# Kernel optimization log

Measured on AMD Instinct MI355X. Metric: run time of the kernel, lower is better.

## Reference

```python
import jax, jax.numpy as jnp
import numpy as np
from jax import lax

K = 3; PAD = 1; STR = 1; DIL = 1; DG = 16; MRM = 10.0


def _conv3(x, w, b):
    y = lax.conv_general_dilated(x, w, (1, 1), ((PAD, PAD), (PAD, PAD)),
                                 dimension_numbers=('NCHW', 'OIHW', 'NCHW'))
    return y + b[None, :, None, None]


def _leaky(x):
    return jnp.where(x >= 0, x, 0.1 * x)


def _bilinear_gather(img, py, px):
    # img: [B, dg, cg, H, W]; py, px: [B, dg, KK, H, W] sampling coords
    B, dg, cg, H, W = img.shape
    KK = py.shape[2]
    y0f = jnp.floor(py); x0f = jnp.floor(px)
    wy = py - y0f; wx = px - x0f          # bilinear fractions (grad flows via py/px)
    y0 = y0f.astype(jnp.int32); x0 = x0f.astype(jnp.int32)
    y1 = y0 + 1; x1 = x0 + 1
    imgf = img.reshape(B * dg, cg, H * W)

    def gather(yi, xi):
        valid = ((yi >= 0) & (yi < H) & (xi >= 0) & (xi < W)).astype(img.dtype)
        idx = jnp.clip(yi, 0, H - 1) * W + jnp.clip(xi, 0, W - 1)
        idxf = idx.reshape(B * dg, KK * H * W)
        v = jax.vmap(lambda im, ix: im[:, ix])(imgf, idxf)  # [B*dg, cg, KK*H*W]
        v = v.reshape(B, dg, cg, KK, H, W)
        return v * valid[:, :, None]  # zero padding outside image

    w00 = ((1 - wy) * (1 - wx))[:, :, None]
    w01 = ((1 - wy) * wx)[:, :, None]
    w10 = (wy * (1 - wx))[:, :, None]
    w11 = (wy * wx)[:, :, None]
    return (gather(y0, x0) * w00 + gather(y0, x1) * w01 +
            gather(y1, x0) * w10 + gather(y1, x1) * w11)


def reference(x, extra_feat, flow, w1, b1, w2, b2, w3, b3, weight):
    B, C, H, W = x.shape
    KK = K * K
    cg = C // DG
    P = DG * KK
    # offset/mask generating convnet
    h = _leaky(_conv3(extra_feat, w1, b1))
    h = _leaky(_conv3(h, w2, b2))
    o = _conv3(h, w3, b3)                       # [B, 3*P, H, W]
    o1, o2, m = jnp.split(o, 3, axis=1)
    off = MRM * jnp.tanh(jnp.concatenate([o1, o2], axis=1))  # [B, 2P, H, W]
    flow_yx = flow[:, ::-1]                      # flip(1): (x,y)->(y,x)
    off = off + jnp.tile(flow_yx, (1, P, 1, 1))
    off = off.reshape(B, DG, KK, 2, H, W)        # pair p=(g,k): channel 2p=y, 2p+1=x
    off_y = off[:, :, :, 0]
    off_x = off[:, :, :, 1]
    mask = jax.nn.sigmoid(m).reshape(B, DG, KK, H, W)

    ki = jnp.arange(KK)
    ky = (ki // K).astype(x.dtype) * DIL - PAD   # kernel row offsets
    kx = (ki % K).astype(x.dtype) * DIL - PAD
    base_h = jnp.arange(H, dtype=x.dtype) * STR
    base_w = jnp.arange(W, dtype=x.dtype) * STR
    py = base_h[None, None, None, :, None] + ky[None, None, :, None, None] + off_y
    px = base_w[None, None, None, None, :] + kx[None, None, :, None, None] + off_x

    img = x.reshape(B, DG, cg, H, W)
    val = _bilinear_gather(img, py, px) * mask[:, :, None]  # [B,dg,cg,KK,H,W]
    wk = weight.reshape(weight.shape[0], DG, cg, KK)
    # modulated deformable conv accumulate (bias=None in original forward)
    return jnp.einsum('bgckhw,ogck->bohw', val, wk)


def setup_inputs() -> dict:
    key = jax.random.key(0)
    ks = jax.random.split(key, 10)
    B, C, H, W = 2, 64, 128, 128
    OFFC = 3 * K * K * DG  # 432
    return {
        'x': jax.random.normal(ks[0], (B, C, H, W), jnp.float32),
        'extra_feat': jax.random.normal(ks[1], (B, 2 * C, H, W), jnp.float32),
        'flow': jax.random.normal(ks[2], (B, 2, H, W), jnp.float32),
        'w1': jax.random.normal(ks[3], (C, 2 * C, 3, 3), jnp.float32) * 0.05,
        'b1': jnp.zeros((C,), jnp.float32),
        'w2': jax.random.normal(ks[4], (C, C, 3, 3), jnp.float32) * 0.05,
        'b2': jnp.zeros((C,), jnp.float32),
        'w3': jax.random.normal(ks[5], (OFFC, C, 3, 3), jnp.float32) * 0.01,
        'b3': jnp.zeros((OFFC,), jnp.float32),
        'weight': jax.random.normal(ks[6], (C, C, 3, 3), jnp.float32) * 0.05,
    }
```

## Files before the change

### kernel.cpp

```cpp
#include <hip/hip_runtime.h>
#include <math.h>

constexpr int B_   = 2;
constexpr int C_   = 64;
constexpr int H_   = 128;
constexpr int W_   = 128;
constexpr int HW_  = H_ * W_;
constexpr int DG_  = 16;
constexpr int KK_  = 9;
constexpr int CG_  = 4;
constexpr int OFFC_ = 3 * KK_ * DG_;
constexpr int R_   = C_ * KK_;
constexpr int WP_  = 130;
constexpr int HWP_ = WP_ * WP_;

typedef _Float16 half8 __attribute__((ext_vector_type(8)));
typedef _Float16 half4 __attribute__((ext_vector_type(4)));
typedef float floatx4 __attribute__((ext_vector_type(4)));

__device__ __forceinline__ void gl_lds16(const _Float16* g, _Float16* l)
{
    __builtin_amdgcn_global_load_lds(
        (const __attribute__((address_space(1))) void*)g,
        (__attribute__((address_space(3))) void*)l, 16, 0, 0);
}

__device__ __forceinline__ int afrag_src(int c)
{
    const int cmf = c >> 6, cq = (c >> 4) & 3, cl = c & 15;
    return (cmf * 16 + cl) * 32 + cq * 8;
}

template <int OC, int CIN>
__global__ __launch_bounds__(256) void prep_wA_k(
    const float* __restrict__ w, _Float16* __restrict__ wA)
{
    constexpr int CH = CIN / 32;
    const int j = blockIdx.x * 256 + threadIdx.x;
    if (j >= 9 * CH * OC * 32) return;
    const int slab = j / (OC * 32);
    const int rem  = j - slab * (OC * 32);
    const int oc   = rem >> 5;
    const int jj   = rem & 31;
    const int t    = slab / CH;
    const int h    = slab - t * CH;
    const int ic   = h * 32 + jj;
    wA[j] = (_Float16)w[(size_t)oc * (CIN * 9) + ic * 9 + t];
}

__global__ __launch_bounds__(256) void prep_wkA_k(
    const float* __restrict__ wk, _Float16* __restrict__ wkA)
{
    const int j = blockIdx.x * 256 + threadIdx.x;
    if (j >= 18 * 64 * 32) return;
    const int s   = j >> 11;
    const int rem = j & 2047;
    const int oc  = rem >> 5;
    const int jj  = rem & 31;
    const int k   = s >> 1;
    const int gc  = (s & 1) * 32 + jj;
    wkA[j] = (_Float16)wk[(size_t)oc * R_ + gc * 9 + k];
}

template <int CC>
__global__ __launch_bounds__(256) void nchw2slabpad_f16_k(
    const float* __restrict__ in, _Float16* __restrict__ outh)
{
    const int pix = blockIdx.x * 256 + threadIdx.x;
    const int b   = blockIdx.y;
    const int yp  = pix >> 7;
    const int xp  = pix & (W_ - 1);
    const float* ib = in + (size_t)b * CC * HW_ + pix;
#pragma unroll
    for (int c0 = 0; c0 < CC; c0 += 8) {
        half8 v;
#pragma unroll
        for (int j = 0; j < 8; ++j)
            v[j] = (_Float16)ib[(size_t)(c0 + j) * HW_];
        const int slab = c0 >> 5;
        *(half8*)&outh[((size_t)(slab * B_ + b) * HWP_
                        + (size_t)(yp + 1) * WP_ + (xp + 1)) * 32 + (c0 & 31)] = v;
    }
}

__global__ __launch_bounds__(256) void nchw2gx_f16_k(
    const float* __restrict__ in, _Float16* __restrict__ outh)
{
    const int pix = blockIdx.x * 256 + threadIdx.x;
    const int b   = blockIdx.y;
    const float* ib = in + (size_t)b * C_ * HW_ + pix;
#pragma unroll
    for (int g = 0; g < DG_; ++g) {
        half4 v;
#pragma unroll
        for (int c = 0; c < 4; ++c)
            v[c] = (_Float16)ib[(size_t)(g * 4 + c) * HW_];
        *(half4*)&outh[((size_t)(b * DG_ + g) * HW_ + pix) * 4] = v;
    }
}

template <int CIN>
__global__ __launch_bounds__(256, 2) void conv12_mfma_k(
    const _Float16* __restrict__ inp, const _Float16* __restrict__ wA,
    const float* __restrict__ bias, _Float16* __restrict__ outp)
{
    constexpr int CH = CIN / 32;
    constexpr int NS = 9 * CH;
    __shared__ __align__(16) _Float16 Asm[2 * 2048];

    const int tid  = threadIdx.x;
    const int lane = tid & 63;
    const int wv   = tid >> 6;
    const int l15  = lane & 15;
    const int quad = lane >> 4;

    const int zx   = blockIdx.x;
    const int row  = zx >> 1;
    const int b    = row >> 7;
    const int y    = row & 127;
    const int px0  = (zx & 1) * 64 + wv * 16;

    const int sA = afrag_src(tid);

    floatx4 acc[4];
#pragma unroll
    for (int mf = 0; mf < 4; ++mf)
        acc[mf] = (floatx4){0.f, 0.f, 0.f, 0.f};

    half8 Bf[2];

    gl_lds16(wA + sA, Asm + tid * 8);
    Bf[0] = *(const half8*)&inp[
        ((size_t)(0 * B_ + b) * HWP_ + (size_t)(y + 0) * WP_
         + (px0 + l15 + 0)) * 32 + quad * 8];
    __syncthreads();

#pragma unroll
    for (int ks = 0; ks < NS; ++ks) {
        const int cur = ks & 1, nxt = cur ^ 1;
        if (ks < NS - 1) {
            const int ks1 = ks + 1;
            const int t = ks1 / CH, h = ks1 % CH;
            const int dy = t / 3, dx = t % 3;
            gl_lds16(wA + (size_t)ks1 * 2048 + sA, Asm + nxt * 2048 + tid * 8);
            Bf[nxt] = *(const half8*)&inp[
                ((size_t)(h * B_ + b) * HWP_ + (size_t)(y + dy) * WP_
                 + (px0 + l15 + dx)) * 32 + quad * 8];
        }
        const _Float16* abase = Asm + cur * 2048 + lane * 8;
#pragma unroll
        for (int mf = 0; mf < 4; ++mf) {
            const half8 afr = *(const half8*)&abase[mf * 512];
            acc[mf] = __builtin_amdgcn_mfma_f32_16x16x32_f16(afr, Bf[cur], acc[mf], 0, 0, 0);
        }
        __syncthreads();
    }

#pragma unroll
    for (int mf = 0; mf < 4; ++mf) {
        const int oc4 = mf * 16 + quad * 4;
        const float4 b4 = *(const float4*)&bias[oc4];
        half4 v4;
#pragma unroll
        for (int reg = 0; reg < 4; ++reg) {
            float r = acc[mf][reg] + ((const float*)&b4)[reg];
            r = (r >= 0.f) ? r : 0.1f * r;
            v4[reg] = (_Float16)r;
        }
        *(half4*)&outp[((size_t)((oc4 >> 5) * B_ + b) * HWP_
                        + (size_t)(y + 1) * WP_ + (px0 + l15 + 1)) * 32 + (oc4 & 31)] = v4;
    }
}

__global__ __launch_bounds__(256, 2) void conv3_mfma_k(
    const _Float16* __restrict__ h2p, const _Float16* __restrict__ w3A,
    const float* __restrict__ bias, const float* __restrict__ flow,
    _Float16* __restrict__ omh)
{
    __shared__ __align__(16) _Float16 Smem[144 * 132];
    _Float16* Asm = Smem;
    _Float16* Lds = Smem;

    const int tid  = threadIdx.x;
    const int lane = tid & 63;
    const int wv   = tid >> 6;
    const int l15  = lane & 15;
    const int quad = lane >> 4;

    const int row = blockIdx.x;
    const int b   = row >> 7;
    const int y   = row & 127;
    const int m0  = blockIdx.y * 144;
    const int px0 = wv * 32;

    const int c0 = wv * 64 + lane;
    const int c1 = 256 + c0;
    const int c2 = 512 + lane;
    const int s0 = afrag_src(c0), s1 = afrag_src(c1), s2 = afrag_src(c2);

    floatx4 acc[9][2];
#pragma unroll
    for (int mf = 0; mf < 9; ++mf)
#pragma unroll
        for (int nf = 0; nf < 2; ++nf)
            acc[mf][nf] = (floatx4){0.f, 0.f, 0.f, 0.f};

    half8 Bf[2][2];

    {
        const _Float16* asrc = w3A + (size_t)m0 * 32;
        gl_lds16(asrc + s0, Asm + c0 * 8);
        gl_lds16(asrc + s1, Asm + c1 * 8);
        if (wv == 0) gl_lds16(asrc + s2, Asm + c2 * 8);
#pragma unroll
        for (int nf = 0; nf < 2; ++nf)
            Bf[0][nf] = *(const half8*)&h2p[
                ((size_t)(0 * B_ + b) * HWP_ + (size_t)(y + 0) * WP_
                 + (px0 + nf * 16 + l15 + 0)) * 32 + quad * 8];
    }
    __syncthreads();

#pragma unroll
    for (int ks = 0; ks < 18; ++ks) {
        const int cur = ks & 1, nxt = cur ^ 1;
        if (ks < 17) {
            const int ks1 = ks + 1;
            const int t = ks1 >> 1, h = ks1 & 1;
            const int dy = t / 3, dx = t % 3;
            const _Float16* asrc = w3A + ((size_t)ks1 * OFFC_ + m0) * 32;
            _Float16* adst = Asm + nxt * 4608;
            gl_lds16(asrc + s0, adst + c0 * 8);
            gl_lds16(asrc + s1, adst + c1 * 8);
            if (wv == 0) gl_lds16(asrc + s2, adst + c2 * 8);
#pragma unroll
            for (int nf = 0; nf < 2; ++nf)
                Bf[nxt][nf] = *(const half8*)&h2p[
                    ((size_t)(h * B_ + b) * HWP_ + (size_t)(y + dy) * WP_
                     + (px0 + nf * 16 + l15 + dx)) * 32 + quad * 8];
        }
        const _Float16* abase = Asm + cur * 4608 + lane * 8;
#pragma unroll
        for (int mf = 0; mf < 9; ++mf) {
            const half8 afr = *(const half8*)&abase[mf * 512];
            acc[mf][0] = __builtin_amdgcn_mfma_f32_16x16x32_f16(afr, Bf[cur][0], acc[mf][0], 0, 0, 0);
            acc[mf][1] = __builtin_amdgcn_mfma_f32_16x16x32_f16(afr, Bf[cur][1], acc[mf][1], 0, 0, 0);
        }
        __syncthreads();
    }

    const bool is_off = (blockIdx.y < 2);
    float flY[2], flX[2];
#pragma unroll
    for (int nf = 0; nf < 2; ++nf) {
        const int px = px0 + nf * 16 + l15;
        if (is_off) {
            flY[nf] = flow[(size_t)(b * 2 + 1) * HW_ + y * W_ + px];
            flX[nf] = flow[(size_t)(b * 2 + 0) * HW_ + y * W_ + px];
        }
    }
#pragma unroll
    for (int mf = 0; mf < 9; ++mf) {
        const float4 b4 = *(const float4*)&bias[m0 + mf * 16 + quad * 4];
#pragma unroll
        for (int nf = 0; nf < 2; ++nf) {
            const int px = px0 + nf * 16 + l15;
#pragma unroll
            for (int reg = 0; reg < 4; ++reg) {
                const int ocl = mf * 16 + quad * 4 + reg;
                float val = acc[mf][nf][reg] + ((const float*)&b4)[reg];
                if (is_off) {
                    const int slot = reg & 1;
                    const float fl = slot ? flX[nf] : flY[nf];
                    const float e = __expf(2.f * val);
                    val = 10.f * (1.f - __fdividef(2.f, e + 1.f)) + fl;
                } else {
                    val = __fdividef(1.f, 1.f + __expf(-val));
                }
                Lds[ocl * 132 + px] = (_Float16)val;
            }
        }
    }
    __syncthreads();

#pragma unroll
    for (int it = 0; it < 18; ++it) {
        const int j4 = it * 256 + tid;
        const int r  = j4 >> 5;
        const int c4 = j4 & 31;
        const int oc = m0 + r;
        int g, k, slot;
        if (oc < 2 * DG_ * KK_) {
            g = oc / 18;
            const int rem = oc - g * 18;
            k = rem >> 1;
            slot = rem & 1;
        } else {
            const int c = oc - 2 * DG_ * KK_;
            g = c / 9;
            k = c - g * 9;
            slot = 2;
        }
        const half4 hv = *(const half4*)&Lds[r * 132 + c4 * 4];
        *(half4*)&omh[((size_t)((b * DG_ * KK_ + g * KK_ + k) * 3 + slot)) * HW_
                      + y * W_ + c4 * 4] = hv;
    }
}

__global__ __launch_bounds__(256) void gather_k(
    const _Float16* __restrict__ xg, const _Float16* __restrict__ omh,
    _Float16* __restrict__ valh)
{
    const int tid = threadIdx.x;
    const int pix = blockIdx.x * 256 + tid;
    const int zy  = blockIdx.y;
    const int b   = zy / KK_;
    const int k   = zy - b * KK_;
    const int yp  = pix >> 7;
    const int xp  = pix & (W_ - 1);
    const float fy = (float)(yp + (k / 3) - 1);
    const float fx = (float)(xp + (k % 3) - 1);

    half4 rec[16];
#pragma unroll
    for (int g = 0; g < DG_; ++g) {
        const size_t obase = ((size_t)((b * DG_ + g) * KK_ + k) * 3) * HW_ + pix;
        const float oy = (float)omh[obase];
        const float ox = (float)omh[obase + HW_];
        const float m  = (float)omh[obase + 2 * HW_];

        const float py = fy + oy;
        const float px = fx + ox;
        const float y0f = floorf(py);
        const float x0f = floorf(px);
        const float wy = py - y0f;
        const float wx = px - x0f;
        const int y0 = (int)y0f, x0 = (int)x0f;
        const int y1 = y0 + 1,  x1 = x0 + 1;
        const bool vy0 = ((unsigned)y0 < (unsigned)H_);
        const bool vy1 = ((unsigned)y1 < (unsigned)H_);
        const bool vx0 = ((unsigned)x0 < (unsigned)W_);
        const bool vx1 = ((unsigned)x1 < (unsigned)W_);
        const float w00 = vy0 && vx0 ? (1.f - wy) * (1.f - wx) : 0.f;
        const float w01 = vy0 && vx1 ? (1.f - wy) * wx         : 0.f;
        const float w10 = vy1 && vx0 ? wy * (1.f - wx)         : 0.f;
        const float w11 = vy1 && vx1 ? wy * wx                 : 0.f;
        const int i00 = (vy0 && vx0) ? y0 * W_ + x0 : 0;
        const int i01 = (vy0 && vx1) ? y0 * W_ + x1 : 0;
        const int i10 = (vy1 && vx0) ? y1 * W_ + x0 : 0;
        const int i11 = (vy1 && vx1) ? y1 * W_ + x1 : 0;

        const _Float16* xb = xg + (size_t)(b * DG_ + g) * HW_ * 4;
        const half4 p00 = *(const half4*)&xb[(size_t)i00 * 4];
        const half4 p01 = *(const half4*)&xb[(size_t)i01 * 4];
        const half4 p10 = *(const half4*)&xb[(size_t)i10 * 4];
        const half4 p11 = *(const half4*)&xb[(size_t)i11 * 4];

        half4 v4;
#pragma unroll
        for (int c = 0; c < CG_; ++c) {
            float v = w00 * (float)p00[c] + w01 * (float)p01[c]
                    + w10 * (float)p10[c] + w11 * (float)p11[c];
            v4[c] = (_Float16)(v * m);
        }
        rec[g] = v4;
    }

    _Float16* r0 = &valh[((size_t)((2 * k) * B_ + b) * HW_ + pix) * 32];
    _Float16* r1 = &valh[((size_t)((2 * k + 1) * B_ + b) * HW_ + pix) * 32];
#pragma unroll
    for (int j = 0; j < 4; ++j) {
        half8 w0, w1;
#pragma unroll
        for (int c = 0; c < 4; ++c) {
            w0[c]     = rec[2 * j][c];
            w0[c + 4] = rec[2 * j + 1][c];
            w1[c]     = rec[8 + 2 * j][c];
            w1[c + 4] = rec[9 + 2 * j][c];
        }
        *(half8*)&r0[j * 8] = w0;
        *(half8*)&r1[j * 8] = w1;
    }
}

__global__ __launch_bounds__(256, 2) void einsum_mfma_k(
    const _Float16* __restrict__ valh, const _Float16* __restrict__ wkA,
    float* __restrict__ out)
{
    __shared__ __align__(16) float Smem[64 * 68];
    _Float16* Asm = (_Float16*)Smem;
    float*    Lds = Smem;

    const int tid  = threadIdx.x;
    const int lane = tid & 63;
    const int wv   = tid >> 6;
    const int l15  = lane & 15;
    const int quad = lane >> 4;

    const int pixg0 = blockIdx.x * 64 + wv * 16;
    const int b     = pixg0 >> 14;
    const int pix0  = pixg0 & (HW_ - 1);

    const int sA = afrag_src(tid);

    floatx4 acc[4];
#pragma unroll
    for (int mf = 0; mf < 4; ++mf)
        acc[mf] = (floatx4){0.f, 0.f, 0.f, 0.f};

    half8 Bf[2];

    gl_lds16(wkA + sA, Asm + tid * 8);
    Bf[0] = *(const half8*)&valh[((size_t)(0 * B_ + b) * HW_ + pix0 + l15) * 32 + quad * 8];
    __syncthreads();

#pragma unroll
    for (int s = 0; s < 18; ++s) {
        const int cur = s & 1, nxt = cur ^ 1;
        if (s < 17) {
            const int s1 = s + 1;
            gl_lds16(wkA + (size_t)s1 * 2048 + sA, Asm + nxt * 2048 + tid * 8);
            Bf[nxt] = *(const half8*)&valh[
                ((size_t)(s1 * B_ + b) * HW_ + pix0 + l15) * 32 + quad * 8];
        }
        const _Float16* abase = Asm + cur * 2048 + lane * 8;
#pragma unroll
        for (int mf = 0; mf < 4; ++mf) {
            const half8 afr = *(const half8*)&abase[mf * 512];
            acc[mf] = __builtin_amdgcn_mfma_f32_16x16x32_f16(afr, Bf[cur], acc[mf], 0, 0, 0);
        }
        __syncthreads();
    }

    const int pxl = wv * 16 + l15;
#pragma unroll
    for (int mf = 0; mf < 4; ++mf)
#pragma unroll
        for (int reg = 0; reg < 4; ++reg)
            Lds[(mf * 16 + quad * 4 + reg) * 68 + pxl] = acc[mf][reg];
    __syncthreads();

    const int pixb = blockIdx.x * 64 & (HW_ - 1);
#pragma unroll
    for (int it = 0; it < 4; ++it) {
        const int j4 = it * 256 + tid;
        const int r  = j4 >> 4;
        const int c4 = j4 & 15;
        float4 v;
        v.x = Lds[r * 68 + c4 * 4 + 0];
        v.y = Lds[r * 68 + c4 * 4 + 1];
        v.z = Lds[r * 68 + c4 * 4 + 2];
        v.w = Lds[r * 68 + c4 * 4 + 3];
        *(float4*)&out[((size_t)(b * C_ + r)) * HW_ + pixb + c4 * 4] = v;
    }
}

extern "C" void kernel_launch(void* const* d_in, const int* in_sizes, int n_in,
                              void* d_out, int out_size, void* d_ws, size_t ws_size,
                              hipStream_t stream)
{
    const float* x    = (const float*)d_in[0];
    const float* ef   = (const float*)d_in[1];
    const float* flow = (const float*)d_in[2];
    const float* w1   = (const float*)d_in[3];
    const float* b1   = (const float*)d_in[4];
    const float* w2   = (const float*)d_in[5];
    const float* b2   = (const float*)d_in[6];
    const float* w3   = (const float*)d_in[7];
    const float* b3   = (const float*)d_in[8];
    const float* wk   = (const float*)d_in[9];
    float* out = (float*)d_out;

    _Float16* omh  = (_Float16*)d_ws;
    _Float16* valh = omh + (size_t)B_ * OFFC_ * HW_;
    _Float16* ef_p = valh + (size_t)18 * B_ * HW_ * 32;
    _Float16* xg   = ef_p + (size_t)4 * B_ * HWP_ * 32;
    _Float16* h1p  = xg + (size_t)B_ * HW_ * 64;
    _Float16* h2p  = h1p + (size_t)2 * B_ * HWP_ * 32;
    _Float16* w1A  = h2p + (size_t)2 * B_ * HWP_ * 32;
    _Float16* w2A  = w1A + 64 * 128 * 9;
    _Float16* w3A  = w2A + 64 * 64 * 9;
    _Float16* wkA  = w3A + OFFC_ * 64 * 9;

    hipMemsetAsync(ef_p, 0, (size_t)4 * B_ * HWP_ * 32 * 2, stream);
    hipMemsetAsync(h1p, 0, (size_t)2 * B_ * HWP_ * 32 * 2, stream);
    hipMemsetAsync(h2p, 0, (size_t)2 * B_ * HWP_ * 32 * 2, stream);

    prep_wA_k<64, 128><<<dim3((64 * 128 * 9 + 255) / 256), 256, 0, stream>>>(w1, w1A);
    prep_wA_k<64, 64><<<dim3((64 * 64 * 9 + 255) / 256), 256, 0, stream>>>(w2, w2A);
    prep_wA_k<OFFC_, 64><<<dim3((OFFC_ * 64 * 9 + 255) / 256), 256, 0, stream>>>(w3, w3A);
    prep_wkA_k<<<dim3((18 * 64 * 32 + 255) / 256), 256, 0, stream>>>(wk, wkA);
    nchw2slabpad_f16_k<128><<<dim3(HW_ / 256, B_), 256, 0, stream>>>(ef, ef_p);
    nchw2gx_f16_k<<<dim3(HW_ / 256, B_), 256, 0, stream>>>(x, xg);

    conv12_mfma_k<128><<<dim3(B_ * H_ * 2), 256, 0, stream>>>(ef_p, w1A, b1, h1p);
    conv12_mfma_k<64><<<dim3(B_ * H_ * 2), 256, 0, stream>>>(h1p, w2A, b2, h2p);
    conv3_mfma_k<<<dim3(B_ * H_, 3), 256, 0, stream>>>(h2p, w3A, b3, flow, omh);

    gather_k<<<dim3(HW_ / 256, B_ * KK_), 256, 0, stream>>>(xg, omh, valh);
    einsum_mfma_k<<<dim3(B_ * HW_ / 64), 256, 0, stream>>>(valh, wkA, out);
}
```

Measured before the change: 204.8 us.

## Cut barriers in conv and einsum kernels via wider stages and resident weights

Conv1 and conv3 now process two K-slices per pipeline stage, which halves the number of __syncthreads barriers and doubles the prefetch depth. Conv2 and the einsum kernel preload all 18 weight slices into LDS up front and drop the per-step barriers, so only the activation loads stay double-buffered. This trades more LDS per block (up to 72 KB, and a larger conv3 staging area) and possibly fewer resident blocks for less synchronisation overhead in the MFMA loops.

```diff
diff --git a/kernel.cpp b/kernel.cpp
--- a/kernel.cpp
+++ b/kernel.cpp
@@ -99,14 +99,11 @@
     }
 }
 
-template <int CIN>
-__global__ __launch_bounds__(256, 2) void conv12_mfma_k(
+__global__ __launch_bounds__(256, 2) void conv1_mfma_k(
     const _Float16* __restrict__ inp, const _Float16* __restrict__ wA,
     const float* __restrict__ bias, _Float16* __restrict__ outp)
 {
-    constexpr int CH = CIN / 32;
-    constexpr int NS = 9 * CH;
-    __shared__ __align__(16) _Float16 Asm[2 * 2048];
+    __shared__ __align__(16) _Float16 Asm[2 * 4096];
 
     const int tid  = threadIdx.x;
     const int lane = tid & 63;
@@ -127,31 +124,42 @@
     for (int mf = 0; mf < 4; ++mf)
         acc[mf] = (floatx4){0.f, 0.f, 0.f, 0.f};
 
-    half8 Bf[2];
-
-    gl_lds16(wA + sA, Asm + tid * 8);
-    Bf[0] = *(const half8*)&inp[
-        ((size_t)(0 * B_ + b) * HWP_ + (size_t)(y + 0) * WP_
-         + (px0 + l15 + 0)) * 32 + quad * 8];
-    __syncthreads();
-
-#pragma unroll
-    for (int ks = 0; ks < NS; ++ks) {
-        const int cur = ks & 1, nxt = cur ^ 1;
-        if (ks < NS - 1) {
-            const int ks1 = ks + 1;
-            const int t = ks1 / CH, h = ks1 % CH;
+    half8 Bf[2][2];
+
+    gl_lds16(wA + 0 * 2048 + sA, Asm + 0 * 2048 + tid * 8);
+    gl_lds16(wA + 1 * 2048 + sA, Asm + 1 * 2048 + tid * 8);
+#pragma unroll
+    for (int j = 0; j < 2; ++j)
+        Bf[0][j] = *(const half8*)&inp[
+            ((size_t)(j * B_ + b) * HWP_ + (size_t)(y + 0) * WP_
+             + (px0 + l15 + 0)) * 32 + quad * 8];
+    __syncthreads();
+
+#pragma unroll
+    for (int p = 0; p < 18; ++p) {
+        const int cur = p & 1, nxt = cur ^ 1;
+        if (p < 17) {
+            const int ks0 = 2 * p + 2;
+            const int t = ks0 >> 2;
+            const int h0 = ks0 & 3;
             const int dy = t / 3, dx = t % 3;
-            gl_lds16(wA + (size_t)ks1 * 2048 + sA, Asm + nxt * 2048 + tid * 8);
-            Bf[nxt] = *(const half8*)&inp[
-                ((size_t)(h * B_ + b) * HWP_ + (size_t)(y + dy) * WP_
-                 + (px0 + l15 + dx)) * 32 + quad * 8];
-        }
-        const _Float16* abase = Asm + cur * 2048 + lane * 8;
-#pragma unroll
-        for (int mf = 0; mf < 4; ++mf) {
-            const half8 afr = *(const half8*)&abase[mf * 512];
-            acc[mf] = __builtin_amdgcn_mfma_f32_16x16x32_f16(afr, Bf[cur], acc[mf], 0, 0, 0);
+#pragma unroll
+            for (int j = 0; j < 2; ++j) {
+                gl_lds16(wA + (size_t)(ks0 + j) * 2048 + sA,
+                         Asm + (nxt * 2 + j) * 2048 + tid * 8);
+                Bf[nxt][j] = *(const half8*)&inp[
+                    ((size_t)((h0 + j) * B_ + b) * HWP_ + (size_t)(y + dy) * WP_
+                     + (px0 + l15 + dx)) * 32 + quad * 8];
+            }
+        }
+#pragma unroll
+        for (int j = 0; j < 2; ++j) {
+            const _Float16* abase = Asm + (cur * 2 + j) * 2048 + lane * 8;
+#pragma unroll
+            for (int mf = 0; mf < 4; ++mf) {
+                const half8 afr = *(const half8*)&abase[mf * 512];
+                acc[mf] = __builtin_amdgcn_mfma_f32_16x16x32_f16(afr, Bf[cur][j], acc[mf], 0, 0, 0);
+            }
         }
         __syncthreads();
     }
@@ -172,14 +180,11 @@
     }
 }
 
-__global__ __launch_bounds__(256, 2) void conv3_mfma_k(
-    const _Float16* __restrict__ h2p, const _Float16* __restrict__ w3A,
-    const float* __restrict__ bias, const float* __restrict__ flow,
-    _Float16* __restrict__ omh)
-{
-    __shared__ __align__(16) _Float16 Smem[144 * 132];
-    _Float16* Asm = Smem;
-    _Float16* Lds = Smem;
+__global__ __launch_bounds__(256, 2) void conv2_mfma_k(
+    const _Float16* __restrict__ inp, const _Float16* __restrict__ wA,
+    const float* __restrict__ bias, _Float16* __restrict__ outp)
+{
+    __shared__ __align__(16) _Float16 Asm[18 * 2048];
 
     const int tid  = threadIdx.x;
     const int lane = tid & 63;
@@ -187,37 +192,27 @@
     const int l15  = lane & 15;
     const int quad = lane >> 4;
 
-    const int row = blockIdx.x;
-    const int b   = row >> 7;
-    const int y   = row & 127;
-    const int m0  = blockIdx.y * 144;
-    const int px0 = wv * 32;
-
-    const int c0 = wv * 64 + lane;
-    const int c1 = 256 + c0;
-    const int c2 = 512 + lane;
-    const int s0 = afrag_src(c0), s1 = afrag_src(c1), s2 = afrag_src(c2);
-
-    floatx4 acc[9][2];
-#pragma unroll
-    for (int mf = 0; mf < 9; ++mf)
-#pragma unroll
-        for (int nf = 0; nf < 2; ++nf)
-            acc[mf][nf] = (floatx4){0.f, 0.f, 0.f, 0.f};
-
-    half8 Bf[2][2];
-
-    {
-        const _Float16* asrc = w3A + (size_t)m0 * 32;
-        gl_lds16(asrc + s0, Asm + c0 * 8);
-        gl_lds16(asrc + s1, Asm + c1 * 8);
-        if (wv == 0) gl_lds16(asrc + s2, Asm + c2 * 8);
-#pragma unroll
-        for (int nf = 0; nf < 2; ++nf)
-            Bf[0][nf] = *(const half8*)&h2p[
-                ((size_t)(0 * B_ + b) * HWP_ + (size_t)(y + 0) * WP_
-                 + (px0 + nf * 16 + l15 + 0)) * 32 + quad * 8];
-    }
+    const int zx   = blockIdx.x;
+    const int row  = zx >> 1;
+    const int b    = row >> 7;
+    const int y    = row & 127;
+    const int px0  = (zx & 1) * 64 + wv * 16;
+
+    const int sA = afrag_src(tid);
+
+#pragma unroll
+    for (int s = 0; s < 18; ++s)
+        gl_lds16(wA + (size_t)s * 2048 + sA, Asm + s * 2048 + tid * 8);
+
+    floatx4 acc[4];
+#pragma unroll
+    for (int mf = 0; mf < 4; ++mf)
+        acc[mf] = (floatx4){0.f, 0.f, 0.f, 0.f};
+
+    half8 Bf[2];
+    Bf[0] = *(const half8*)&inp[
+        ((size_t)(0 * B_ + b) * HWP_ + (size_t)(y + 0) * WP_
+         + (px0 + l15 + 0)) * 32 + quad * 8];
     __syncthreads();
 
 #pragma unroll
@@ -227,23 +222,116 @@
             const int ks1 = ks + 1;
             const int t = ks1 >> 1, h = ks1 & 1;
             const int dy = t / 3, dx = t % 3;
-            const _Float16* asrc = w3A + ((size_t)ks1 * OFFC_ + m0) * 32;
-            _Float16* adst = Asm + nxt * 4608;
+            Bf[nxt] = *(const half8*)&inp[
+                ((size_t)(h * B_ + b) * HWP_ + (size_t)(y + dy) * WP_
+                 + (px0 + l15 + dx)) * 32 + quad * 8];
+        }
+        const _Float16* abase = Asm + ks * 2048 + lane * 8;
+#pragma unroll
+        for (int mf = 0; mf < 4; ++mf) {
+            const half8 afr = *(const half8*)&abase[mf * 512];
+            acc[mf] = __builtin_amdgcn_mfma_f32_16x16x32_f16(afr, Bf[cur], acc[mf], 0, 0, 0);
+        }
+    }
+
+#pragma unroll
+    for (int mf = 0; mf < 4; ++mf) {
+        const int oc4 = mf * 16 + quad * 4;
+        const float4 b4 = *(const float4*)&bias[oc4];
+        half4 v4;
+#pragma unroll
+        for (int reg = 0; reg < 4; ++reg) {
+            float r = acc[mf][reg] + ((const float*)&b4)[reg];
+            r = (r >= 0.f) ? r : 0.1f * r;
+            v4[reg] = (_Float16)r;
+        }
+        *(half4*)&outp[((size_t)((oc4 >> 5) * B_ + b) * HWP_
+                        + (size_t)(y + 1) * WP_ + (px0 + l15 + 1)) * 32 + (oc4 & 31)] = v4;
+    }
+}
+
+__global__ __launch_bounds__(256, 2) void conv3_mfma_k(
+    const _Float16* __restrict__ h2p, const _Float16* __restrict__ w3A,
+    const float* __restrict__ bias, const float* __restrict__ flow,
+    _Float16* __restrict__ omh)
+{
+    __shared__ __align__(16) _Float16 Smem[144 * 132];
+    _Float16* Asm = Smem;
+    _Float16* Lds = Smem;
+
+    const int tid  = threadIdx.x;
+    const int lane = tid & 63;
+    const int wv   = tid >> 6;
+    const int l15  = lane & 15;
+    const int quad = lane >> 4;
+
+    const int row = blockIdx.x;
+    const int b   = row >> 7;
+    const int y   = row & 127;
+    const int m0  = blockIdx.y * 144;
+    const int px0 = wv * 32;
+
+    const int c0 = wv * 64 + lane;
+    const int c1 = 256 + c0;
+    const int c2 = 512 + lane;
+    const int s0 = afrag_src(c0), s1 = afrag_src(c1), s2 = afrag_src(c2);
+
+    floatx4 acc[9][2];
+#pragma unroll
+    for (int mf = 0; mf < 9; ++mf)
+#pragma unroll
+        for (int nf = 0; nf < 2; ++nf)
+            acc[mf][nf] = (floatx4){0.f, 0.f, 0.f, 0.f};
+
+    half8 Bf[2][2][2];
+
+    {
+#pragma unroll
+        for (int j = 0; j < 2; ++j) {
+            const _Float16* asrc = w3A + ((size_t)j * OFFC_ + m0) * 32;
+            _Float16* adst = Asm + j * 4608;
             gl_lds16(asrc + s0, adst + c0 * 8);
             gl_lds16(asrc + s1, adst + c1 * 8);
             if (wv == 0) gl_lds16(asrc + s2, adst + c2 * 8);
 #pragma unroll
             for (int nf = 0; nf < 2; ++nf)
-                Bf[nxt][nf] = *(const half8*)&h2p[
-                    ((size_t)(h * B_ + b) * HWP_ + (size_t)(y + dy) * WP_
-                     + (px0 + nf * 16 + l15 + dx)) * 32 + quad * 8];
-        }
-        const _Float16* abase = Asm + cur * 4608 + lane * 8;
-#pragma unroll
-        for (int mf = 0; mf < 9; ++mf) {
-            const half8 afr = *(const half8*)&abase[mf * 512];
-            acc[mf][0] = __builtin_amdgcn_mfma_f32_16x16x32_f16(afr, Bf[cur][0], acc[mf][0], 0, 0, 0);
-            acc[mf][1] = __builtin_amdgcn_mfma_f32_16x16x32_f16(afr, Bf[cur][1], acc[mf][1], 0, 0, 0);
+                Bf[0][j][nf] = *(const half8*)&h2p[
+                    ((size_t)(j * B_ + b) * HWP_ + (size_t)(y + 0) * WP_
+                     + (px0 + nf * 16 + l15 + 0)) * 32 + quad * 8];
+        }
+    }
+    __syncthreads();
+
+#pragma unroll
+    for (int p = 0; p < 9; ++p) {
+        const int cur = p & 1, nxt = cur ^ 1;
+        if (p < 8) {
+            const int t = p + 1;
+            const int dy = t / 3, dx = t % 3;
+#pragma unroll
+            for (int j = 0; j < 2; ++j) {
+                const int ks = 2 * t + j;
+                const _Float16* asrc = w3A + ((size_t)ks * OFFC_ + m0) * 32;
+                _Float16* adst = Asm + (nxt * 2 + j) * 4608;
+                gl_lds16(asrc + s0, adst + c0 * 8);
+                gl_lds16(asrc + s1, adst + c1 * 8);
+                if (wv == 0) gl_lds16(asrc + s2, adst + c2 * 8);
+#pragma unroll
+                for (int nf = 0; nf < 2; ++nf)
+                    Bf[nxt][j][nf] = *(const half8*)&h2p[
+                        ((size_t)(j * B_ + b) * HWP_ + (size_t)(y + dy) * WP_
+                         + (px0 + nf * 16 + l15 + dx)) * 32 + quad * 8];
+            }
+        }
+#pragma unroll
+        for (int j = 0; j < 2; ++j) {
+            const _Float16* abase = Asm + (cur * 2 + j) * 4608 + lane * 8;
+#pragma unroll
+            for (int mf = 0; mf < 9; ++mf) {
+                const half8 afr = *(const half8*)&abase[mf * 512];
+                acc[mf][0] = __builtin_amdgcn_mfma_f32_16x16x32_f16(afr, Bf[cur][j][0], acc[mf][0], 0, 0, 0);
+                acc[mf][1] = __builtin_amdgcn_mfma_f32_16x16x32_f16(afr, Bf[cur][j][1], acc[mf][1], 0, 0, 0);
+            }
         }
         __syncthreads();
     }
@@ -386,9 +474,8 @@
     const _Float16* __restrict__ valh, const _Float16* __restrict__ wkA,
     float* __restrict__ out)
 {
-    __shared__ __align__(16) float Smem[64 * 68];
-    _Float16* Asm = (_Float16*)Smem;
-    float*    Lds = Smem;
+    __shared__ __align__(16) _Float16 Smem[18 * 2048];
+    float* Lds = (float*)Smem;
 
     const int tid  = threadIdx.x;
     const int lane = tid & 63;
@@ -402,14 +489,16 @@
 
     const int sA = afrag_src(tid);
 
+#pragma unroll
+    for (int s = 0; s < 18; ++s)
+        gl_lds16(wkA + (size_t)s * 2048 + sA, Smem + s * 2048 + tid * 8);
+
     floatx4 acc[4];
 #pragma unroll
     for (int mf = 0; mf < 4; ++mf)
         acc[mf] = (floatx4){0.f, 0.f, 0.f, 0.f};
 
     half8 Bf[2];
-
-    gl_lds16(wkA + sA, Asm + tid * 8);
     Bf[0] = *(const half8*)&valh[((size_t)(0 * B_ + b) * HW_ + pix0 + l15) * 32 + quad * 8];
     __syncthreads();
 
@@ -418,18 +507,17 @@
         const int cur = s & 1, nxt = cur ^ 1;
         if (s < 17) {
             const int s1 = s + 1;
-            gl_lds16(wkA + (size_t)s1 * 2048 + sA, Asm + nxt * 2048 + tid * 8);
             Bf[nxt] = *(const half8*)&valh[
                 ((size_t)(s1 * B_ + b) * HW_ + pix0 + l15) * 32 + quad * 8];
         }
-        const _Float16* abase = Asm + cur * 2048 + lane * 8;
+        const _Float16* abase = Smem + s * 2048 + lane * 8;
 #pragma unroll
         for (int mf = 0; mf < 4; ++mf) {
             const half8 afr = *(const half8*)&abase[mf * 512];
             acc[mf] = __builtin_amdgcn_mfma_f32_16x16x32_f16(afr, Bf[cur], acc[mf], 0, 0, 0);
         }
-        __syncthreads();
-    }
+    }
+    __syncthreads();
 
     const int pxl = wv * 16 + l15;
 #pragma unroll
@@ -492,8 +580,8 @@
     nchw2slabpad_f16_k<128><<<dim3(HW_ / 256, B_), 256, 0, stream>>>(ef, ef_p);
     nchw2gx_f16_k<<<dim3(HW_ / 256, B_), 256, 0, stream>>>(x, xg);
 
-    conv12_mfma_k<128><<<dim3(B_ * H_ * 2), 256, 0, stream>>>(ef_p, w1A, b1, h1p);
-    conv12_mfma_k<64><<<dim3(B_ * H_ * 2), 256, 0, stream>>>(h1p, w2A, b2, h2p);
+    conv1_mfma_k<<<dim3(B_ * H_ * 2), 256, 0, stream>>>(ef_p, w1A, b1, h1p);
+    conv2_mfma_k<<<dim3(B_ * H_ * 2), 256, 0, stream>>>(h1p, w2A, b2, h2p);
     conv3_mfma_k<<<dim3(B_ * H_, 3), 256, 0, stream>>>(h2p, w3A, b3, flow, omh);
 
     gather_k<<<dim3(HW_ / 256, B_ * KK_), 256, 0, stream>>>(xg, omh, valh);
```

Result: no change. 206.3 us (+0.7%).
